# Kernel optimization log

Hardware: AMD Instinct MI355X
Metric: run time of the kernel (lower is better)

## Reference

```python
import jax, jax.numpy as jnp
import numpy as np

B, F, A, H = 131072, 32, 8, 64  # batch, n_features, n_actions, hidden

def setup_inputs() -> dict:
    key = jax.random.key(0)
    k = jax.random.split(key, 6)
    return {
        "f_t": jax.random.normal(k[0], (B, F), dtype=jnp.float32),
        "a_t": jax.random.normal(k[1], (B, A), dtype=jnp.float32),
        "W1": jax.random.normal(k[2], (F, F + A, H), dtype=jnp.float32) * 0.1,
        "b1": jax.random.normal(k[3], (F, H), dtype=jnp.float32) * 0.1,
        "W2": jax.random.normal(k[4], (F, H), dtype=jnp.float32) * 0.1,
        "b2": jax.random.normal(k[5], (F,), dtype=jnp.float32) * 0.1,
    }

def reference(f_t, a_t, W1, b1, W2, b2):
    # fa_t: [B, F+A] shared input to all F submodels
    fa_t = jnp.concatenate((f_t, a_t), axis=1)
    # Batched grouped-GEMM over the F independent submodels.
    h = jax.nn.relu(jnp.einsum('bi,fih->bfh', fa_t, W1) + b1)  # [B, F, H]
    f_t1 = jnp.einsum('bfh,fh->bf', h, W2) + b2                 # [B, F]
    # skip_connection=True
    return f_t1 + f_t
```

## Files before the change

kernel.cpp:

```cpp
#include <hip/hip_runtime.h>

#define B_TOTAL 131072
#define NF 32
#define NA 8
#define NH 64

using frag_ab = __attribute__((ext_vector_type(8))) short;
using frag_cd = __attribute__((ext_vector_type(4))) float;
typedef int v2i __attribute__((ext_vector_type(2)));

__device__ __forceinline__ unsigned short f2bf(float x) {
  unsigned u = __float_as_uint(x);
  u = (u + 0x7FFFu + ((u >> 16) & 1u)) >> 16;
  return (unsigned short)u;
}

__global__ void pack_w1_kernel(const float* __restrict__ W1, const float* __restrict__ b1,
                               unsigned short* __restrict__ w1p) {
  int idx = blockIdx.x * 256 + threadIdx.x;
  int j = idx & 7, l = (idx >> 3) & 63, nt = (idx >> 9) & 3, ks = (idx >> 11) & 1, f = idx >> 12;
  int g = l >> 4, c = l & 15;
  int i = ks * 32 + g * 8 + j;
  int h = nt * 16 + c;
  float v = 0.0f;
  if (i < NF + NA)            v = W1[(f * (NF + NA) + i) * NH + h];
  else if (i == NF + NA)      v = b1[f * NH + h];
  w1p[idx] = f2bf(v);
}

__global__ void pack_w2_kernel(const float* __restrict__ W2, float* __restrict__ w2p) {
  int idx = blockIdx.x * 256 + threadIdx.x;
  int j = idx & 3, rt = (idx >> 2) & 3, g2 = (idx >> 4) & 3, f = idx >> 6;
  w2p[idx] = W2[f * NH + g2 * 4 + j + 16 * rt];
}

template <int PAT>
__device__ __forceinline__ float swz_xor_add(float v) {
  int m = __builtin_amdgcn_ds_swizzle(__float_as_int(v), PAT);
  return v + __int_as_float(m);
}

__device__ __forceinline__ float xor32_add(float v) {
  v2i p = __builtin_amdgcn_permlane32_swap(__float_as_int(v), __float_as_int(v), false, false);
  return __int_as_float(p.x) + __int_as_float(p.y);
}

__global__ __launch_bounds__(256, 2) void fused_mlp_kernel(
    const float* __restrict__ ft, const float* __restrict__ at,
    const unsigned short* __restrict__ w1p, const float* __restrict__ w2p,
    const float* __restrict__ b2, float* __restrict__ out) {
  __shared__ __align__(16) unsigned short wlds[2][16384];

  const int t = threadIdx.x;
  const int wv = t >> 6;
  const int l = t & 63;
  const int g2 = (l >> 4) & 3;
  const int c = l & 15;
  const long rowb = (long)blockIdx.x * 256 + wv * 64;

  {
    const unsigned short* src = w1p + t * 8;
#pragma unroll
    for (int k = 0; k < 8; ++k)
      __builtin_amdgcn_global_load_lds((const __attribute__((address_space(1))) void*)(src + k * 2048),
                                       (__attribute__((address_space(3))) void*)(&wlds[0][k * 2048 + t * 8]), 16, 0, 0);
  }

  frag_ab bfr[4][2];
#pragma unroll
  for (int bt = 0; bt < 4; ++bt) {
    const long b = rowb + bt * 16 + c;
    float tmp[8];
    *(float4*)tmp       = *(const float4*)(ft + b * NF + g2 * 8);
    *(float4*)(tmp + 4) = *(const float4*)(ft + b * NF + g2 * 8 + 4);
    frag_ab f0;
#pragma unroll
    for (int j = 0; j < 8; ++j) f0[j] = (short)f2bf(tmp[j]);
    bfr[bt][0] = f0;

    float av[8];
    *(float4*)av       = *(const float4*)(at + b * NA);
    *(float4*)(av + 4) = *(const float4*)(at + b * NA + 4);
    frag_ab f1;
#pragma unroll
    for (int j = 0; j < 8; ++j) {
      unsigned short bias = (j == 0) ? (unsigned short)0x3F80 : (unsigned short)0;
      unsigned short v = (g2 == 0) ? f2bf(av[j]) : ((g2 == 1) ? bias : (unsigned short)0);
      f1[j] = (short)v;
    }
    bfr[bt][1] = f1;
  }

  const frag_cd zero4 = {0.f, 0.f, 0.f, 0.f};
  const float4* w2p4 = (const float4*)w2p;
  const float4* b2v4 = (const float4*)b2;

  for (int r = 0; r < 8; ++r) {
    __syncthreads();

    if (r < 7) {
      const unsigned short* src = w1p + (r + 1) * 16384 + t * 8;
#pragma unroll
      for (int k = 0; k < 8; ++k)
        __builtin_amdgcn_global_load_lds((const __attribute__((address_space(1))) void*)(src + k * 2048),
                                         (__attribute__((address_space(3))) void*)(&wlds[(r + 1) & 1][k * 2048 + t * 8]), 16, 0, 0);
    }

    const unsigned short* buf = wlds[r & 1];
    float res[4];

#pragma unroll
    for (int fo = 0; fo < 4; ++fo) {
      const int f = r * 4 + fo;

      float4 w2v[4];
#pragma unroll
      for (int rt = 0; rt < 4; ++rt) w2v[rt] = w2p4[(f * 4 + g2) * 4 + rt];

      float s[4] = {0.f, 0.f, 0.f, 0.f};
#pragma unroll
      for (int rt = 0; rt < 4; ++rt) {
        frag_ab wf0 = *(const frag_ab*)&buf[(((fo * 2 + 0) * 4 + rt) * 64 + l) * 8];
        frag_ab wf1 = *(const frag_ab*)&buf[(((fo * 2 + 1) * 4 + rt) * 64 + l) * 8];
#pragma unroll
        for (int bt = 0; bt < 4; ++bt) {
          frag_cd a = __builtin_amdgcn_mfma_f32_16x16x32_bf16(wf0, bfr[bt][0], zero4, 0, 0, 0);
          a = __builtin_amdgcn_mfma_f32_16x16x32_bf16(wf1, bfr[bt][1], a, 0, 0, 0);
          s[bt] += fmaxf(a[0], 0.f) * w2v[rt].x;
          s[bt] += fmaxf(a[1], 0.f) * w2v[rt].y;
          s[bt] += fmaxf(a[2], 0.f) * w2v[rt].z;
          s[bt] += fmaxf(a[3], 0.f) * w2v[rt].w;
        }
      }

      float sb[4];
#pragma unroll
      for (int bt = 0; bt < 4; ++bt) {
        float v = swz_xor_add<0x401F>(s[bt]);
        sb[bt] = xor32_add(v);
      }
      float r01 = (g2 & 1) ? sb[1] : sb[0];
      float r23 = (g2 & 1) ? sb[3] : sb[2];
      res[fo] = (g2 & 2) ? r23 : r01;
    }

    const long row = rowb + l;
    float4 bb = b2v4[r];
    float4 fv = *(const float4*)(ft + row * NF + r * 4);
    float4 o;
    o.x = res[0] + bb.x + fv.x;
    o.y = res[1] + bb.y + fv.y;
    o.z = res[2] + bb.z + fv.z;
    o.w = res[3] + bb.w + fv.w;
    *(float4*)(out + row * NF + r * 4) = o;
  }
}

extern "C" void kernel_launch(void* const* d_in, const int* in_sizes, int n_in,
                              void* d_out, int out_size, void* d_ws, size_t ws_size,
                              hipStream_t stream) {
  const float* ft = (const float*)d_in[0];
  const float* at = (const float*)d_in[1];
  const float* W1 = (const float*)d_in[2];
  const float* b1 = (const float*)d_in[3];
  const float* W2 = (const float*)d_in[4];
  const float* b2 = (const float*)d_in[5];
  float* out = (float*)d_out;

  unsigned short* w1p = (unsigned short*)d_ws;
  float* w2p = (float*)((char*)d_ws + (1u << 18));

  pack_w1_kernel<<<512, 256, 0, stream>>>(W1, b1, w1p);
  pack_w2_kernel<<<8, 256, 0, stream>>>(W2, w2p);
  fused_mlp_kernel<<<B_TOTAL / 256, 256, 0, stream>>>(ft, at, w1p, w2p, b2, out);
}
```

Before: 61.39 us.

## Switch to 32x32x16 MFMA tiles with trimmed K padding and packed FMA epilogue

Replaces the 16x16x32 bf16 MFMA tiling with 32x32x16 tiles. The padded K dimension shrinks from 64 to 48, which removes a third of the wasted MFMA work and cuts weight bytes staged into LDS. The W1/W2 packing layouts are rebuilt to match. The second-layer reduction now uses packed v_pk_fma_f32 and needs only one cross-lane swap step. Output writes are deferred into a 32-entry register array and stored once at the end, which raises register pressure under launch_bounds(256,2).

```diff
diff --git a/kernel.cpp b/kernel.cpp
--- a/kernel.cpp
+++ b/kernel.cpp
@@ -6,8 +6,9 @@
 #define NH 64
 
 using frag_ab = __attribute__((ext_vector_type(8))) short;
-using frag_cd = __attribute__((ext_vector_type(4))) float;
-typedef int v2i __attribute__((ext_vector_type(2)));
+using f32x16  = __attribute__((ext_vector_type(16))) float;
+typedef int   v2i __attribute__((ext_vector_type(2)));
+typedef float v2f __attribute__((ext_vector_type(2)));
 
 __device__ __forceinline__ unsigned short f2bf(float x) {
   unsigned u = __float_as_uint(x);
@@ -18,26 +19,27 @@
 __global__ void pack_w1_kernel(const float* __restrict__ W1, const float* __restrict__ b1,
                                unsigned short* __restrict__ w1p) {
   int idx = blockIdx.x * 256 + threadIdx.x;
-  int j = idx & 7, l = (idx >> 3) & 63, nt = (idx >> 9) & 3, ks = (idx >> 11) & 1, f = idx >> 12;
-  int g = l >> 4, c = l & 15;
-  int i = ks * 32 + g * 8 + j;
-  int h = nt * 16 + c;
+  int j = idx & 7, l = (idx >> 3) & 63, tq = idx >> 9;
+  int q = tq % 6, f = tq / 6;
+  int ht = q / 3, kt = q % 3;
+  int h = ht * 32 + (l & 31);
+  int i = kt * 16 + ((l >> 5) << 3) + j;
   float v = 0.0f;
-  if (i < NF + NA)            v = W1[(f * (NF + NA) + i) * NH + h];
-  else if (i == NF + NA)      v = b1[f * NH + h];
+  if (i < NF + NA)       v = W1[(f * (NF + NA) + i) * NH + h];
+  else if (i == NF + NA) v = b1[f * NH + h];
   w1p[idx] = f2bf(v);
 }
 
 __global__ void pack_w2_kernel(const float* __restrict__ W2, float* __restrict__ w2p) {
   int idx = blockIdx.x * 256 + threadIdx.x;
-  int j = idx & 3, rt = (idx >> 2) & 3, g2 = (idx >> 4) & 3, f = idx >> 6;
-  w2p[idx] = W2[f * NH + g2 * 4 + j + 16 * rt];
+  int r = idx & 15, ht = (idx >> 4) & 1, g = (idx >> 5) & 1, f = idx >> 6;
+  w2p[idx] = W2[f * NH + ht * 32 + (r & 3) + 8 * (r >> 2) + 4 * g];
 }
 
-template <int PAT>
-__device__ __forceinline__ float swz_xor_add(float v) {
-  int m = __builtin_amdgcn_ds_swizzle(__float_as_int(v), PAT);
-  return v + __int_as_float(m);
+__device__ __forceinline__ v2f pk_fma(v2f a, v2f b, v2f c) {
+  v2f d;
+  asm("v_pk_fma_f32 %0, %1, %2, %3" : "=v"(d) : "v"(a), "v"(b), "v"(c));
+  return d;
 }
 
 __device__ __forceinline__ float xor32_add(float v) {
@@ -49,110 +51,123 @@
     const float* __restrict__ ft, const float* __restrict__ at,
     const unsigned short* __restrict__ w1p, const float* __restrict__ w2p,
     const float* __restrict__ b2, float* __restrict__ out) {
-  __shared__ __align__(16) unsigned short wlds[2][16384];
+  __shared__ __align__(16) unsigned short wlds[2][12288];
 
   const int t = threadIdx.x;
   const int wv = t >> 6;
   const int l = t & 63;
-  const int g2 = (l >> 4) & 3;
-  const int c = l & 15;
+  const int g = l >> 5;
+  const int lc = l & 31;
   const long rowb = (long)blockIdx.x * 256 + wv * 64;
 
   {
     const unsigned short* src = w1p + t * 8;
 #pragma unroll
-    for (int k = 0; k < 8; ++k)
+    for (int k = 0; k < 6; ++k)
       __builtin_amdgcn_global_load_lds((const __attribute__((address_space(1))) void*)(src + k * 2048),
                                        (__attribute__((address_space(3))) void*)(&wlds[0][k * 2048 + t * 8]), 16, 0, 0);
   }
 
-  frag_ab bfr[4][2];
+  frag_ab bfr[2][3];
 #pragma unroll
-  for (int bt = 0; bt < 4; ++bt) {
-    const long b = rowb + bt * 16 + c;
+  for (int bt = 0; bt < 2; ++bt) {
+    const long b = rowb + bt * 32 + lc;
+    const float* fr = ft + b * NF;
     float tmp[8];
-    *(float4*)tmp       = *(const float4*)(ft + b * NF + g2 * 8);
-    *(float4*)(tmp + 4) = *(const float4*)(ft + b * NF + g2 * 8 + 4);
-    frag_ab f0;
 #pragma unroll
-    for (int j = 0; j < 8; ++j) f0[j] = (short)f2bf(tmp[j]);
-    bfr[bt][0] = f0;
-
-    float av[8];
-    *(float4*)av       = *(const float4*)(at + b * NA);
-    *(float4*)(av + 4) = *(const float4*)(at + b * NA + 4);
-    frag_ab f1;
+    for (int kt = 0; kt < 2; ++kt) {
+      *(float4*)tmp       = *(const float4*)(fr + kt * 16 + g * 8);
+      *(float4*)(tmp + 4) = *(const float4*)(fr + kt * 16 + g * 8 + 4);
+      frag_ab fb;
+#pragma unroll
+      for (int j = 0; j < 8; ++j) fb[j] = (short)f2bf(tmp[j]);
+      bfr[bt][kt] = fb;
+    }
+    *(float4*)tmp       = *(const float4*)(at + b * NA);
+    *(float4*)(tmp + 4) = *(const float4*)(at + b * NA + 4);
+    frag_ab fb;
 #pragma unroll
     for (int j = 0; j < 8; ++j) {
       unsigned short bias = (j == 0) ? (unsigned short)0x3F80 : (unsigned short)0;
-      unsigned short v = (g2 == 0) ? f2bf(av[j]) : ((g2 == 1) ? bias : (unsigned short)0);
-      f1[j] = (short)v;
+      fb[j] = (short)((g == 0) ? f2bf(tmp[j]) : bias);
     }
-    bfr[bt][1] = f1;
+    bfr[bt][2] = fb;
   }
 
-  const frag_cd zero4 = {0.f, 0.f, 0.f, 0.f};
-  const float4* w2p4 = (const float4*)w2p;
-  const float4* b2v4 = (const float4*)b2;
+  const f32x16 zero16 = {0.f,0.f,0.f,0.f,0.f,0.f,0.f,0.f,0.f,0.f,0.f,0.f,0.f,0.f,0.f,0.f};
+  float res[NF];
 
   for (int r = 0; r < 8; ++r) {
     __syncthreads();
 
     if (r < 7) {
-      const unsigned short* src = w1p + (r + 1) * 16384 + t * 8;
+      const unsigned short* src = w1p + (r + 1) * 12288 + t * 8;
 #pragma unroll
-      for (int k = 0; k < 8; ++k)
+      for (int k = 0; k < 6; ++k)
         __builtin_amdgcn_global_load_lds((const __attribute__((address_space(1))) void*)(src + k * 2048),
                                          (__attribute__((address_space(3))) void*)(&wlds[(r + 1) & 1][k * 2048 + t * 8]), 16, 0, 0);
     }
 
     const unsigned short* buf = wlds[r & 1];
-    float res[4];
 
 #pragma unroll
     for (int fo = 0; fo < 4; ++fo) {
       const int f = r * 4 + fo;
 
-      float4 w2v[4];
+      frag_ab wf[2][3];
 #pragma unroll
-      for (int rt = 0; rt < 4; ++rt) w2v[rt] = w2p4[(f * 4 + g2) * 4 + rt];
+      for (int ht = 0; ht < 2; ++ht)
+#pragma unroll
+        for (int kt = 0; kt < 3; ++kt)
+          wf[ht][kt] = *(const frag_ab*)&buf[((fo * 6 + ht * 3 + kt) * 64 + l) * 8];
 
-      float s[4] = {0.f, 0.f, 0.f, 0.f};
+      float4 wq[8];
+      const float4* wp = (const float4*)w2p + (f * 2 + g) * 8;
 #pragma unroll
-      for (int rt = 0; rt < 4; ++rt) {
-        frag_ab wf0 = *(const frag_ab*)&buf[(((fo * 2 + 0) * 4 + rt) * 64 + l) * 8];
-        frag_ab wf1 = *(const frag_ab*)&buf[(((fo * 2 + 1) * 4 + rt) * 64 + l) * 8];
+      for (int q = 0; q < 8; ++q) wq[q] = wp[q];
+
+      float sb[2];
 #pragma unroll
-        for (int bt = 0; bt < 4; ++bt) {
-          frag_cd a = __builtin_amdgcn_mfma_f32_16x16x32_bf16(wf0, bfr[bt][0], zero4, 0, 0, 0);
-          a = __builtin_amdgcn_mfma_f32_16x16x32_bf16(wf1, bfr[bt][1], a, 0, 0, 0);
-          s[bt] += fmaxf(a[0], 0.f) * w2v[rt].x;
-          s[bt] += fmaxf(a[1], 0.f) * w2v[rt].y;
-          s[bt] += fmaxf(a[2], 0.f) * w2v[rt].z;
-          s[bt] += fmaxf(a[3], 0.f) * w2v[rt].w;
+      for (int bt = 0; bt < 2; ++bt) {
+        f32x16 a0 = zero16, a1 = zero16;
+#pragma unroll
+        for (int kt = 0; kt < 3; ++kt) {
+          a0 = __builtin_amdgcn_mfma_f32_32x32x16_bf16(wf[0][kt], bfr[bt][kt], a0, 0, 0, 0);
+          a1 = __builtin_amdgcn_mfma_f32_32x32x16_bf16(wf[1][kt], bfr[bt][kt], a1, 0, 0, 0);
         }
+        v2f ps0 = {0.f, 0.f}, ps1 = {0.f, 0.f};
+#pragma unroll
+        for (int rq = 0; rq < 4; ++rq) {
+          float4 w0 = wq[rq], w1 = wq[4 + rq];
+          v2f m;
+          m[0] = fmaxf(a0[rq * 4 + 0], 0.f); m[1] = fmaxf(a0[rq * 4 + 1], 0.f);
+          ps0 = pk_fma(m, (v2f){w0.x, w0.y}, ps0);
+          m[0] = fmaxf(a0[rq * 4 + 2], 0.f); m[1] = fmaxf(a0[rq * 4 + 3], 0.f);
+          ps0 = pk_fma(m, (v2f){w0.z, w0.w}, ps0);
+          m[0] = fmaxf(a1[rq * 4 + 0], 0.f); m[1] = fmaxf(a1[rq * 4 + 1], 0.f);
+          ps1 = pk_fma(m, (v2f){w1.x, w1.y}, ps1);
+          m[0] = fmaxf(a1[rq * 4 + 2], 0.f); m[1] = fmaxf(a1[rq * 4 + 3], 0.f);
+          ps1 = pk_fma(m, (v2f){w1.z, w1.w}, ps1);
+        }
+        float s = (ps0[0] + ps0[1]) + (ps1[0] + ps1[1]);
+        sb[bt] = xor32_add(s);
       }
+      res[f] = g ? sb[1] : sb[0];
+    }
+  }
 
-      float sb[4];
+  const long row = rowb + l;
+  const float4* fr = (const float4*)(ft + row * NF);
+  const float4* bb = (const float4*)b2;
+  float4* op = (float4*)(out + row * NF);
 #pragma unroll
-      for (int bt = 0; bt < 4; ++bt) {
-        float v = swz_xor_add<0x401F>(s[bt]);
-        sb[bt] = xor32_add(v);
-      }
-      float r01 = (g2 & 1) ? sb[1] : sb[0];
-      float r23 = (g2 & 1) ? sb[3] : sb[2];
-      res[fo] = (g2 & 2) ? r23 : r01;
-    }
-
-    const long row = rowb + l;
-    float4 bb = b2v4[r];
-    float4 fv = *(const float4*)(ft + row * NF + r * 4);
-    float4 o;
-    o.x = res[0] + bb.x + fv.x;
-    o.y = res[1] + bb.y + fv.y;
-    o.z = res[2] + bb.z + fv.z;
-    o.w = res[3] + bb.w + fv.w;
-    *(float4*)(out + row * NF + r * 4) = o;
+  for (int q = 0; q < 8; ++q) {
+    float4 x = fr[q], bv = bb[q], o;
+    o.x = res[q * 4 + 0] + bv.x + x.x;
+    o.y = res[q * 4 + 1] + bv.y + x.y;
+    o.z = res[q * 4 + 2] + bv.z + x.z;
+    o.w = res[q * 4 + 3] + bv.w + x.w;
+    op[q] = o;
   }
 }
 
@@ -170,7 +185,7 @@
   unsigned short* w1p = (unsigned short*)d_ws;
   float* w2p = (float*)((char*)d_ws + (1u << 18));
 
-  pack_w1_kernel<<<512, 256, 0, stream>>>(W1, b1, w1p);
-  pack_w2_kernel<<<8, 256, 0, stream>>>(W2, w2p);
+  pack_w1_kernel<<<384, 256, 0, stream>>>(W1, b1, w1p);
+  pack_w2_kernel<<<16, 256, 0, stream>>>(W2, w2p);
   fused_mlp_kernel<<<B_TOTAL / 256, 256, 0, stream>>>(ft, at, w1p, w2p, b2, out);
 }
```

Result: no change. 61.41 us (+0.0%).
